# Kernel tuning notes

Measured on AMD Instinct MI355X. Metric: run time of the kernel, lower is better.

## Reference

```python
import jax, jax.numpy as jnp
import numpy as np

NB = 2        # trm_num_blocks
H = 4         # trm_num_heads
D = 128       # trm_hidden_dim
L = 512
B = 1
PAD = 0
NEG = jnp.float32(-2**32 + 1)


def _ln(x, g, b, eps=1e-8):
    m = x.mean(-1, keepdims=True)
    v = x.var(-1, keepdims=True)
    return (x - m) / jnp.sqrt(v + eps) * g + b


def setup_inputs() -> dict:
    key = jax.random.key(0)
    ks = jax.random.split(key, 16)
    s = 0.02
    inp = {
        "log_seqs": jax.random.randint(ks[0], (B, L), 0, 1000),
        "seqs": jax.random.normal(ks[1], (B, L, D), jnp.float32),
        "time_matrix_K": jax.random.normal(ks[2], (B, L, L, D), jnp.float32),
        # per-block stacked params [NB, ...]
        "Wq": jax.random.normal(ks[3], (NB, D, D), jnp.float32) * s,
        "bq": jnp.zeros((NB, D), jnp.float32),
        "Wk": jax.random.normal(ks[4], (NB, D, D), jnp.float32) * s,
        "bk": jnp.zeros((NB, D), jnp.float32),
        "Wv": jax.random.normal(ks[5], (NB, D, D), jnp.float32) * s,
        "bv": jnp.zeros((NB, D), jnp.float32),
        "Wt": jax.random.normal(ks[6], (NB, D, D), jnp.float32) * s,
        "bt": jnp.zeros((NB, D), jnp.float32),
        "Wtp": jax.random.normal(ks[7], (NB, D, 1), jnp.float32) * s,
        "btp": jnp.zeros((NB, 1), jnp.float32),
        "ln1_g": jnp.ones((NB, D), jnp.float32),
        "ln1_b": jnp.zeros((NB, D), jnp.float32),
        "ln2_g": jnp.ones((NB, D), jnp.float32),
        "ln2_b": jnp.zeros((NB, D), jnp.float32),
        "W1": jax.random.normal(ks[8], (NB, D, D), jnp.float32) * s,
        "b1": jnp.zeros((NB, D), jnp.float32),
        "W2": jax.random.normal(ks[9], (NB, D, D), jnp.float32) * s,
        "b2": jnp.zeros((NB, D), jnp.float32),
        "lnf_g": jnp.ones((D,), jnp.float32),
        "lnf_b": jnp.zeros((D,), jnp.float32),
    }
    return inp


def reference(log_seqs, seqs, time_matrix_K, Wq, bq, Wk, bk, Wv, bv, Wt, bt,
              Wtp, btp, ln1_g, ln1_b, ln2_g, ln2_b, W1, b1, W2, b2, lnf_g, lnf_b):
    hd = D // H
    pad = (log_seqs == PAD)                     # [B, L] True at padding
    keep = (~pad)[..., None].astype(seqs.dtype)  # [B, L, 1]
    seqs = seqs * keep
    causal = ~jnp.tril(jnp.ones((L, L), bool))  # True above diagonal (masked)
    # combined mask [1, B, L, L]: pad query rows OR non-causal entries
    mask = pad[None, :, :, None] | causal[None, None, :, :]

    attn_ws = []
    for i in range(NB):
        Q = _ln(seqs, ln1_g[i], ln1_b[i])
        q = Q @ Wq[i] + bq[i]
        k = seqs @ Wk[i] + bk[i]
        v = seqs @ Wv[i] + bv[i]
        # head-major layout [H, B, L, hd] (matches torch split+cat along dim 0)
        qh = q.reshape(B, L, H, hd).transpose(2, 0, 1, 3)
        kh = k.reshape(B, L, H, hd).transpose(2, 0, 1, 3)
        vh = v.reshape(B, L, H, hd).transpose(2, 0, 1, 3)
        scores = jnp.einsum('hbqd,hbkd->hbqk', qh, kh)  # [H, B, L, L]
        # time bias: sigmoid(proj(relu(W_t t))) in (0,1); log is negative
        tw = jax.nn.sigmoid(
            (jax.nn.relu(time_matrix_K @ Wt[i] + bt[i]) @ Wtp[i] + btp[i]).squeeze(-1)
        )                                             # [B, L, L]
        scores = (scores + jnp.log(tw)) / jnp.float32(hd) ** 0.5
        scores = jnp.where(mask, NEG, scores)
        w = jax.nn.softmax(scores, axis=-1)           # dropout is identity (eval)
        attn_ws.append(w.reshape(H * B, L, L))
        out = jnp.einsum('hbqk,hbkd->hbqd', w, vh).transpose(1, 2, 0, 3).reshape(B, L, D)
        seqs = Q + out
        x = _ln(seqs, ln2_g[i], ln2_b[i])
        y = jax.nn.relu(x @ W1[i] + b1[i]) @ W2[i] + b2[i]
        seqs = (x + y) * keep                         # FFN residual adds post-LN x
    log_feats = _ln(seqs, lnf_g, lnf_b)
    return (log_feats, tuple(attn_ws))
```

## Files before the change

kernel.cpp:

```cpp
#include <hip/hip_runtime.h>

#define L 512
#define D 128
#define H 4
#define HD 32
#define XLD 132

typedef __bf16 bf16x8 __attribute__((ext_vector_type(8)));
typedef float  f32x4  __attribute__((ext_vector_type(4)));

__device__ __forceinline__ unsigned short bfbits(float v){
  __bf16 h = (__bf16)v; unsigned short u; __builtin_memcpy(&u, &h, 2); return u;
}
__device__ __forceinline__ bf16x8 cvt8(float4 a0, float4 a1){
  bf16x8 r;
  r[0] = (__bf16)a0.x; r[1] = (__bf16)a0.y; r[2] = (__bf16)a0.z; r[3] = (__bf16)a0.w;
  r[4] = (__bf16)a1.x; r[5] = (__bf16)a1.y; r[6] = (__bf16)a1.z; r[7] = (__bf16)a1.w;
  return r;
}

__device__ __forceinline__ void write_qA(unsigned short* qA, int row, int c, float v){
  int qt = row >> 4, m = row & 15;
  int h = c >> 5, cc = c & 31;
  qA[(((qt * 4 + h) * 64) + (cc >> 3) * 16 + m) * 8 + (cc & 7)] = bfbits(v);
}
__device__ __forceinline__ void write_kB(unsigned short* kB, int row, int c, float v){
  int h = c >> 5, cc = c & 31;
  int nt = row >> 4;
  kB[((h * 32 + nt) * 64 + (cc >> 3) * 16 + (row & 15)) * 8 + (cc & 7)] = bfbits(v);
}
__device__ __forceinline__ void write_vB(unsigned short* vB, int row, int c, float v){
  int h = c >> 5, cc = c & 31;
  int kk = row >> 5, qv = (row >> 3) & 3, jv = row & 7;
  int nt = cc >> 4;
  vB[(((h * 16 + kk) * 2 + nt) * 64 + qv * 16 + (cc & 15)) * 8 + jv] = bfbits(v);
}

__device__ __forceinline__ void row_stats16(const float (*buf)[XLD], int tid,
                                            float* mean_s, float* rstd_s){
  int row_l = tid >> 4, seg = tid & 15;
  const float* p = &buf[row_l][seg * 8];
  float4 f0 = *(const float4*)p, f1 = *(const float4*)(p + 4);
  float sum = f0.x + f0.y + f0.z + f0.w + f1.x + f1.y + f1.z + f1.w;
  float sq  = f0.x*f0.x + f0.y*f0.y + f0.z*f0.z + f0.w*f0.w
            + f1.x*f1.x + f1.y*f1.y + f1.z*f1.z + f1.w*f1.w;
#pragma unroll
  for (int o = 1; o < 16; o <<= 1){ sum += __shfl_xor(sum, o); sq += __shfl_xor(sq, o); }
  if (seg == 0){
    float mn = sum * (1.f / 128.f);
    mean_s[row_l] = mn;
    rstd_s[row_l] = rsqrtf(fmaxf(sq * (1.f / 128.f) - mn * mn, 0.f) + 1e-8f);
  }
}

__device__ __forceinline__ void build_afr(const float (*buf)[XLD], int lane, bf16x8* afr){
  int m = lane & 15, quad = lane >> 4;
#pragma unroll
  for (int k0 = 0; k0 < 4; ++k0){
    const float* p = &buf[m][k0 * 32 + quad * 8];
    afr[k0] = cvt8(*(const float4*)p, *(const float4*)(p + 4));
  }
}
__device__ __forceinline__ void build_afr_ln(const float (*buf)[XLD], int lane,
    const float* mean_s, const float* rstd_s,
    const float* __restrict__ g, const float* __restrict__ b, bf16x8* afr){
  int m = lane & 15, quad = lane >> 4;
  float mn = mean_s[m], rs = rstd_s[m];
#pragma unroll
  for (int k0 = 0; k0 < 4; ++k0){
    int c0 = k0 * 32 + quad * 8;
    const float* p = &buf[m][c0];
    float4 a0 = *(const float4*)p, a1 = *(const float4*)(p + 4);
    float q[8];
    q[0]=(a0.x-mn)*rs*g[c0+0]+b[c0+0]; q[1]=(a0.y-mn)*rs*g[c0+1]+b[c0+1];
    q[2]=(a0.z-mn)*rs*g[c0+2]+b[c0+2]; q[3]=(a0.w-mn)*rs*g[c0+3]+b[c0+3];
    q[4]=(a1.x-mn)*rs*g[c0+4]+b[c0+4]; q[5]=(a1.y-mn)*rs*g[c0+5]+b[c0+5];
    q[6]=(a1.z-mn)*rs*g[c0+6]+b[c0+6]; q[7]=(a1.w-mn)*rs*g[c0+7]+b[c0+7];
    bf16x8 r;
    r[0]=(__bf16)q[0]; r[1]=(__bf16)q[1]; r[2]=(__bf16)q[2]; r[3]=(__bf16)q[3];
    r[4]=(__bf16)q[4]; r[5]=(__bf16)q[5]; r[6]=(__bf16)q[6]; r[7]=(__bf16)q[7];
    afr[k0] = r;
  }
}

__global__ void k_prep(const float* __restrict__ Wt,
                       const float* __restrict__ Wq, const float* __restrict__ Wk,
                       const float* __restrict__ Wv, const float* __restrict__ W1,
                       const float* __restrict__ W2,
                       unsigned short* __restrict__ bfg, unsigned short* __restrict__ wf){
  int idx = blockIdx.x * 256 + threadIdx.x;
  if (idx < 32768){
    int jj   = idx & 7;
    int lane = (idx >> 3) & 63;
    int k0   = (idx >> 9) & 3;
    int nt   = idx >> 11;
    int d    = k0 * 32 + (lane >> 4) * 8 + jj;
    int col  = (nt & 7) * 16 + (lane & 15);
    int blk  = nt >> 3;
    bfg[idx] = bfbits(Wt[blk * D * D + d * D + col]);
  } else {
    int i2 = idx - 32768;
    int jj = i2 & 7, lane = (i2 >> 3) & 63, k0 = (i2 >> 9) & 3, nt = (i2 >> 11) & 7;
    int mat = i2 >> 14;
    int blk = mat / 5, m5 = mat % 5;
    const float* W = (m5 == 0 ? Wq : m5 == 1 ? Wk : m5 == 2 ? Wv : m5 == 3 ? W1 : W2)
                     + blk * D * D;
    int d = k0 * 32 + (lane >> 4) * 8 + jj;
    int col = nt * 16 + (lane & 15);
    wf[i2] = bfbits(W[d * D + col]);
  }
}

__global__ __launch_bounds__(256, 4) void k_timebias(
    const float* __restrict__ T, const unsigned short* __restrict__ bfg,
    const float* __restrict__ bt, const float* __restrict__ wtp,
    const float* __restrict__ btp, float* __restrict__ logtw){
  __shared__ __align__(16) unsigned short bsh[16384];
  __shared__ float bts[128], wtps[128];
  int tid = threadIdx.x;
  int lane = tid & 63, w = tid >> 6;
  int quad = lane >> 4, m = lane & 15;
  const bf16x8* bls = (const bf16x8*)bsh;
  int wbase = blockIdx.x * 256 + w * 64;

  bf16x8 afr[4][4];
#pragma unroll
  for (int mt = 0; mt < 4; ++mt){
    const float* tp = T + (size_t)(wbase + mt * 16 + m) * D + quad * 8;
#pragma unroll
    for (int k0 = 0; k0 < 4; ++k0){
      float4 f0 = *(const float4*)(tp + k0 * 32);
      float4 f1 = *(const float4*)(tp + k0 * 32 + 4);
      afr[mt][k0] = cvt8(f0, f1);
    }
  }

#pragma unroll
  for (int blk = 0; blk < 2; ++blk){
    if (blk) __syncthreads();
    {
      const uint4* g = (const uint4*)(bfg + blk * 16384);
      uint4* s = (uint4*)bsh;
#pragma unroll
      for (int i = 0; i < 8; ++i) s[tid + i * 256] = g[tid + i * 256];
      if (tid < 128){ bts[tid] = bt[blk * 128 + tid]; wtps[tid] = wtp[blk * 128 + tid]; }
    }
    __syncthreads();

    f32x4 rs[4] = {{0,0,0,0},{0,0,0,0},{0,0,0,0},{0,0,0,0}};
#pragma unroll
    for (int ntl = 0; ntl < 8; ++ntl){
      f32x4 acc[4] = {{0,0,0,0},{0,0,0,0},{0,0,0,0},{0,0,0,0}};
#pragma unroll
      for (int k0 = 0; k0 < 4; ++k0){
        bf16x8 b = bls[(ntl * 4 + k0) * 64 + lane];
#pragma unroll
        for (int mt = 0; mt < 4; ++mt)
          acc[mt] = __builtin_amdgcn_mfma_f32_16x16x32_bf16(afr[mt][k0], b, acc[mt], 0, 0, 0);
      }
      float btv = bts[ntl * 16 + m];
      float wtv = wtps[ntl * 16 + m];
#pragma unroll
      for (int mt = 0; mt < 4; ++mt)
#pragma unroll
        for (int r = 0; r < 4; ++r)
          rs[mt][r] += fmaxf(acc[mt][r] + btv, 0.f) * wtv;
    }
#pragma unroll
    for (int mt = 0; mt < 4; ++mt)
#pragma unroll
      for (int r = 0; r < 4; ++r){
        float v = rs[mt][r];
        v += __shfl_xor(v, 1); v += __shfl_xor(v, 2);
        v += __shfl_xor(v, 4); v += __shfl_xor(v, 8);
        rs[mt][r] = v;
      }
    if (m == 0){
      float bp = btp[blk];
      float* out = logtw + blk * (L * L);
#pragma unroll
      for (int mt = 0; mt < 4; ++mt){
        float4 o;
        float s0 = rs[mt][0] + bp; o.x = -logf(1.f + expf(-s0));
        float s1 = rs[mt][1] + bp; o.y = -logf(1.f + expf(-s1));
        float s2 = rs[mt][2] + bp; o.z = -logf(1.f + expf(-s2));
        float s3 = rs[mt][3] + bp; o.w = -logf(1.f + expf(-s3));
        *(float4*)(out + wbase + mt * 16 + quad * 4) = o;
      }
    }
  }
}

__global__ __launch_bounds__(256) void k_qkv_m(
    const float* __restrict__ src, const int* __restrict__ ls, int domask,
    const float* __restrict__ g1, const float* __restrict__ b1,
    const unsigned short* __restrict__ wf, int matq,
    const float* __restrict__ bq, const float* __restrict__ bk,
    const float* __restrict__ bv,
    float* __restrict__ Q, unsigned short* __restrict__ qA,
    unsigned short* __restrict__ kB, unsigned short* __restrict__ vB){
  __shared__ float xs[16][XLD];
  __shared__ float mean_s[16], rstd_s[16];
  __shared__ float g1s[128], b1s[128];
  int tid = threadIdx.x, rowbase = blockIdx.x * 16;
  int row_l = tid >> 4, seg = tid & 15;

  const float* sp = src + (rowbase + row_l) * D + seg * 8;
  float4 f0 = *(const float4*)sp, f1 = *(const float4*)(sp + 4);
  if (domask && ls[rowbase + row_l] == 0){
    f0 = make_float4(0,0,0,0); f1 = make_float4(0,0,0,0);
  }
  *(float4*)&xs[row_l][seg * 8] = f0;
  *(float4*)&xs[row_l][seg * 8 + 4] = f1;
  if (tid < 128){ g1s[tid] = g1[tid]; b1s[tid] = b1[tid]; }
  __syncthreads();
  row_stats16(xs, tid, mean_s, rstd_s);
  __syncthreads();

  {
    float mn = mean_s[row_l], rs = rstd_s[row_l];
    float* qp = Q + (rowbase + row_l) * D + seg * 8;
    float4 o0, o1;
    int c0 = seg * 8;
    o0.x=(f0.x-mn)*rs*g1s[c0+0]+b1s[c0+0]; o0.y=(f0.y-mn)*rs*g1s[c0+1]+b1s[c0+1];
    o0.z=(f0.z-mn)*rs*g1s[c0+2]+b1s[c0+2]; o0.w=(f0.w-mn)*rs*g1s[c0+3]+b1s[c0+3];
    o1.x=(f1.x-mn)*rs*g1s[c0+4]+b1s[c0+4]; o1.y=(f1.y-mn)*rs*g1s[c0+5]+b1s[c0+5];
    o1.z=(f1.z-mn)*rs*g1s[c0+6]+b1s[c0+6]; o1.w=(f1.w-mn)*rs*g1s[c0+7]+b1s[c0+7];
    *(float4*)qp = o0; *(float4*)(qp + 4) = o1;
  }

  int lane = tid & 63, w = tid >> 6;
  int quad = lane >> 4, mcol = lane & 15;
  bf16x8 afrQ[4], afrX[4];
  build_afr_ln(xs, lane, mean_s, rstd_s, g1s, b1s, afrQ);
  build_afr(xs, lane, afrX);

#pragma unroll
  for (int jl = 0; jl < 6; ++jl){
    int j = w * 6 + jl;
    int mat = j >> 3, nt = j & 7;
    const bf16x8* wfb = (const bf16x8*)wf + ((size_t)(matq + mat) * 8 + nt) * 4 * 64;
    f32x4 acc = {0, 0, 0, 0};
#pragma unroll
    for (int k0 = 0; k0 < 4; ++k0)
      acc = __builtin_amdgcn_mfma_f32_16x16x32_bf16(mat == 0 ? afrQ[k0] : afrX[k0],
                                                    wfb[k0 * 64 + lane], acc, 0, 0, 0);
    int c = nt * 16 + mcol;
    float bias = (mat == 0 ? bq : mat == 1 ? bk : bv)[c];
#pragma unroll
    for (int r = 0; r < 4; ++r){
      int row = rowbase + quad * 4 + r;
      float v = acc[r] + bias;
      if (mat == 0) write_qA(qA, row, c, v);
      else if (mat == 1) write_kB(kB, row, c, v);
      else write_vB(vB, row, c, v);
    }
  }
}

__global__ __launch_bounds__(256) void k_attn(
    const unsigned short* __restrict__ qA, const unsigned short* __restrict__ kB,
    const unsigned short* __restrict__ vB, const float* __restrict__ logtw,
    const int* __restrict__ ls, const float* __restrict__ Q,
    float* __restrict__ wout, float* __restrict__ xr){
  __shared__ __align__(16) unsigned short pa[16 * 64 * 8];
  __shared__ float pvp[4][2][64][4];
  __shared__ float smax[4][16], ssum[4][16];
  int qt = blockIdx.x >> 2, h = blockIdx.x & 3;
  int tid = threadIdx.x, lane = tid & 63, w = tid >> 6;
  int quad = lane >> 4, mcol = lane & 15;
  const float RS = 0.17677669529663687f;

  bf16x8 qf = ((const bf16x8*)qA)[(qt * 4 + h) * 64 + lane];

  f32x4 acc[8];
#pragma unroll
  for (int nt8 = 0; nt8 < 8; ++nt8){
    bf16x8 bf = ((const bf16x8*)kB)[(h * 32 + w * 8 + nt8) * 64 + lane];
    f32x4 z = {0, 0, 0, 0};
    acc[nt8] = __builtin_amdgcn_mfma_f32_16x16x32_bf16(qf, bf, z, 0, 0, 0);
  }

  float e[8][4];
  float mx4[4] = {-3e38f, -3e38f, -3e38f, -3e38f};
#pragma unroll
  for (int nt8 = 0; nt8 < 8; ++nt8){
    int col = w * 128 + nt8 * 16 + mcol;
#pragma unroll
    for (int r = 0; r < 4; ++r){
      int row = qt * 16 + quad * 4 + r;
      float sv = (acc[nt8][r] + logtw[row * L + col]) * RS;
      sv = (col <= row) ? sv : -3e38f;
      e[nt8][r] = sv;
      mx4[r] = fmaxf(mx4[r], sv);
    }
  }
#pragma unroll
  for (int r = 0; r < 4; ++r){
    float v = mx4[r];
    v = fmaxf(v, __shfl_xor(v, 1)); v = fmaxf(v, __shfl_xor(v, 2));
    v = fmaxf(v, __shfl_xor(v, 4)); v = fmaxf(v, __shfl_xor(v, 8));
    mx4[r] = v;
  }
  if (mcol == 0){
#pragma unroll
    for (int r = 0; r < 4; ++r) smax[w][quad * 4 + r] = mx4[r];
  }
  __syncthreads();
  float mxr[4], sum4[4] = {0, 0, 0, 0};
#pragma unroll
  for (int r = 0; r < 4; ++r){
    int rr = quad * 4 + r;
    mxr[r] = fmaxf(fmaxf(smax[0][rr], smax[1][rr]), fmaxf(smax[2][rr], smax[3][rr]));
  }
#pragma unroll
  for (int nt8 = 0; nt8 < 8; ++nt8)
#pragma unroll
    for (int r = 0; r < 4; ++r){
      float sv = e[nt8][r];
      float ev = (sv > -1e38f) ? expf(sv - mxr[r]) : 0.f;
      e[nt8][r] = ev;
      sum4[r] += ev;
    }
#pragma unroll
  for (int r = 0; r < 4; ++r){
    float v = sum4[r];
    v += __shfl_xor(v, 1); v += __shfl_xor(v, 2);
    v += __shfl_xor(v, 4); v += __shfl_xor(v, 8);
    sum4[r] = v;
  }
  if (mcol == 0){
#pragma unroll
    for (int r = 0; r < 4; ++r) ssum[w][quad * 4 + r] = sum4[r];
  }
  __syncthreads();
  float inv[4]; int padr[4];
#pragma unroll
  for (int r = 0; r < 4; ++r){
    int rr = quad * 4 + r;
    inv[r] = 1.f / (ssum[0][rr] + ssum[1][rr] + ssum[2][rr] + ssum[3][rr]);
    padr[r] = (ls[qt * 16 + rr] == 0);
  }
#pragma unroll
  for (int nt8 = 0; nt8 < 8; ++nt8){
    int col = w * 128 + nt8 * 16 + mcol;
    int kk = col >> 5, qk = (col >> 3) & 3, jj = col & 7;
#pragma unroll
    for (int r = 0; r < 4; ++r){
      int rl = quad * 4 + r;
      float wv = padr[r] ? (1.f / 512.f) : e[nt8][r] * inv[r];
      wout[h * (L * L) + (qt * 16 + rl) * L + col] = wv;
      pa[(kk * 64 + qk * 16 + rl) * 8 + jj] = bfbits(wv);
    }
  }

  f32x4 pacc[2] = {{0,0,0,0},{0,0,0,0}};
#pragma unroll
  for (int kk4 = 0; kk4 < 4; ++kk4){
    int kk = w * 4 + kk4;
    bf16x8 af = ((const bf16x8*)pa)[kk * 64 + lane];
#pragma unroll
    for (int nt = 0; nt < 2; ++nt){
      bf16x8 bf = ((const bf16x8*)vB)[((h * 16 + kk) * 2 + nt) * 64 + lane];
      pacc[nt] = __builtin_amdgcn_mfma_f32_16x16x32_bf16(af, bf, pacc[nt], 0, 0, 0);
    }
  }
#pragma unroll
  for (int nt = 0; nt < 2; ++nt)
#pragma unroll
    for (int r = 0; r < 4; ++r) pvp[w][nt][lane][r] = pacc[nt][r];
  __syncthreads();
  if (w < 2){
    int nt = w;
#pragma unroll
    for (int r = 0; r < 4; ++r){
      float o = pvp[0][nt][lane][r] + pvp[1][nt][lane][r]
              + pvp[2][nt][lane][r] + pvp[3][nt][lane][r];
      int row = qt * 16 + quad * 4 + r;
      int cg = h * HD + nt * 16 + mcol;
      xr[row * D + cg] = Q[row * D + cg] + o;
    }
  }
}

__global__ __launch_bounds__(256) void k_ffn_m(
    const float* __restrict__ xr, const int* __restrict__ ls,
    const float* __restrict__ g2, const float* __restrict__ b2,
    const unsigned short* __restrict__ wf, int mat1,
    const float* __restrict__ b1f, const float* __restrict__ b2f,
    int fuse_qkv, const float* __restrict__ g1, const float* __restrict__ b1,
    int matq, const float* __restrict__ bq, const float* __restrict__ bk,
    const float* __restrict__ bv,
    float* __restrict__ Q, unsigned short* __restrict__ qA,
    unsigned short* __restrict__ kB, unsigned short* __restrict__ vB,
    int fuse_lnf, const float* __restrict__ lg, const float* __restrict__ lb,
    float* __restrict__ lf){
  __shared__ float xs[16][XLD];
  __shared__ float x2s[16][XLD];
  __shared__ float y1s[16][XLD];
  __shared__ float xos[16][XLD];
  __shared__ float mean_s[16], rstd_s[16];
  __shared__ float gs[128], bs[128];
  int tid = threadIdx.x, rowbase = blockIdx.x * 16;
  int row_l = tid >> 4, seg = tid & 15;
  int lane = tid & 63, w = tid >> 6;
  int quad = lane >> 4, mcol = lane & 15;

  {
    const float* sp = xr + (rowbase + row_l) * D + seg * 8;
    *(float4*)&xs[row_l][seg * 8] = *(const float4*)sp;
    *(float4*)&xs[row_l][seg * 8 + 4] = *(const float4*)(sp + 4);
    if (tid < 128){ gs[tid] = g2[tid]; bs[tid] = b2[tid]; }
  }
  __syncthreads();
  row_stats16(xs, tid, mean_s, rstd_s);
  __syncthreads();
  {
    float mn = mean_s[row_l], rs = rstd_s[row_l];
#pragma unroll
    for (int i = 0; i < 8; ++i){
      int c = seg * 8 + i;
      x2s[row_l][c] = (xs[row_l][c] - mn) * rs * gs[c] + bs[c];
    }
  }
  __syncthreads();

  bf16x8 afr[4];
  build_afr(x2s, lane, afr);
#pragma unroll
  for (int jl = 0; jl < 2; ++jl){
    int nt = w * 2 + jl;
    const bf16x8* wfb = (const bf16x8*)wf + ((size_t)mat1 * 8 + nt) * 4 * 64;
    f32x4 acc = {0, 0, 0, 0};
#pragma unroll
    for (int k0 = 0; k0 < 4; ++k0)
      acc = __builtin_amdgcn_mfma_f32_16x16x32_bf16(afr[k0], wfb[k0 * 64 + lane], acc, 0, 0, 0);
    int c = nt * 16 + mcol;
    float bias = b1f[c];
#pragma unroll
    for (int r = 0; r < 4; ++r)
      y1s[quad * 4 + r][c] = fmaxf(acc[r] + bias, 0.f);
  }
  __syncthreads();

  build_afr(y1s, lane, afr);
#pragma unroll
  for (int jl = 0; jl < 2; ++jl){
    int nt = w * 2 + jl;
    const bf16x8* wfb = (const bf16x8*)wf + ((size_t)(mat1 + 1) * 8 + nt) * 4 * 64;
    f32x4 acc = {0, 0, 0, 0};
#pragma unroll
    for (int k0 = 0; k0 < 4; ++k0)
      acc = __builtin_amdgcn_mfma_f32_16x16x32_bf16(afr[k0], wfb[k0 * 64 + lane], acc, 0, 0, 0);
    int c = nt * 16 + mcol;
    float bias = b2f[c];
#pragma unroll
    for (int r = 0; r < 4; ++r){
      int rl = quad * 4 + r;
      float kp = (ls[rowbase + rl] != 0) ? 1.f : 0.f;
      xos[rl][c] = (x2s[rl][c] + acc[r] + bias) * kp;
    }
  }
  __syncthreads();

  if (fuse_qkv){
    if (tid < 128){ gs[tid] = g1[tid]; bs[tid] = b1[tid]; }
    row_stats16(xos, tid, mean_s, rstd_s);
    __syncthreads();
    {
      float mn = mean_s[row_l], rs = rstd_s[row_l];
      float* qp = Q + (rowbase + row_l) * D + seg * 8;
      float4 o0, o1;
      int c0 = seg * 8;
      o0.x=(xos[row_l][c0+0]-mn)*rs*gs[c0+0]+bs[c0+0];
      o0.y=(xos[row_l][c0+1]-mn)*rs*gs[c0+1]+bs[c0+1];
      o0.z=(xos[row_l][c0+2]-mn)*rs*gs[c0+2]+bs[c0+2];
      o0.w=(xos[row_l][c0+3]-mn)*rs*gs[c0+3]+bs[c0+3];
      o1.x=(xos[row_l][c0+4]-mn)*rs*gs[c0+4]+bs[c0+4];
      o1.y=(xos[row_l][c0+5]-mn)*rs*gs[c0+5]+bs[c0+5];
      o1.z=(xos[row_l][c0+6]-mn)*rs*gs[c0+6]+bs[c0+6];
      o1.w=(xos[row_l][c0+7]-mn)*rs*gs[c0+7]+bs[c0+7];
      *(float4*)qp = o0; *(float4*)(qp + 4) = o1;
    }
    bf16x8 afrQ[4], afrX[4];
    build_afr_ln(xos, lane, mean_s, rstd_s, gs, bs, afrQ);
    build_afr(xos, lane, afrX);
#pragma unroll
    for (int jl = 0; jl < 6; ++jl){
      int j = w * 6 + jl;
      int mat = j >> 3, nt = j & 7;
      const bf16x8* wfb = (const bf16x8*)wf + ((size_t)(matq + mat) * 8 + nt) * 4 * 64;
      f32x4 acc = {0, 0, 0, 0};
#pragma unroll
      for (int k0 = 0; k0 < 4; ++k0)
        acc = __builtin_amdgcn_mfma_f32_16x16x32_bf16(mat == 0 ? afrQ[k0] : afrX[k0],
                                                      wfb[k0 * 64 + lane], acc, 0, 0, 0);
      int c = nt * 16 + mcol;
      float bias = (mat == 0 ? bq : mat == 1 ? bk : bv)[c];
#pragma unroll
      for (int r = 0; r < 4; ++r){
        int row = rowbase + quad * 4 + r;
        float v = acc[r] + bias;
        if (mat == 0) write_qA(qA, row, c, v);
        else if (mat == 1) write_kB(kB, row, c, v);
        else write_vB(vB, row, c, v);
      }
    }
  }

  if (fuse_lnf){
    if (tid < 128){ gs[tid] = lg[tid]; bs[tid] = lb[tid]; }
    row_stats16(xos, tid, mean_s, rstd_s);
    __syncthreads();
    float mn = mean_s[row_l], rs = rstd_s[row_l];
    float* op = lf + (rowbase + row_l) * D + seg * 8;
    float4 o0, o1;
    int c0 = seg * 8;
    o0.x=(xos[row_l][c0+0]-mn)*rs*gs[c0+0]+bs[c0+0];
    o0.y=(xos[row_l][c0+1]-mn)*rs*gs[c0+1]+bs[c0+1];
    o0.z=(xos[row_l][c0+2]-mn)*rs*gs[c0+2]+bs[c0+2];
    o0.w=(xos[row_l][c0+3]-mn)*rs*gs[c0+3]+bs[c0+3];
    o1.x=(xos[row_l][c0+4]-mn)*rs*gs[c0+4]+bs[c0+4];
    o1.y=(xos[row_l][c0+5]-mn)*rs*gs[c0+5]+bs[c0+5];
    o1.z=(xos[row_l][c0+6]-mn)*rs*gs[c0+6]+bs[c0+6];
    o1.w=(xos[row_l][c0+7]-mn)*rs*gs[c0+7]+bs[c0+7];
    *(float4*)op = o0; *(float4*)(op + 4) = o1;
  }
}

extern "C" void kernel_launch(void* const* d_in, const int* in_sizes, int n_in,
                              void* d_out, int out_size, void* d_ws, size_t ws_size,
                              hipStream_t stream){
  const int*   ls   = (const int*)d_in[0];
  const float* seqs = (const float*)d_in[1];
  const float* T    = (const float*)d_in[2];
  const float* Wq   = (const float*)d_in[3];
  const float* bq   = (const float*)d_in[4];
  const float* Wk   = (const float*)d_in[5];
  const float* bk   = (const float*)d_in[6];
  const float* Wv   = (const float*)d_in[7];
  const float* bv   = (const float*)d_in[8];
  const float* Wt   = (const float*)d_in[9];
  const float* bt   = (const float*)d_in[10];
  const float* Wtp  = (const float*)d_in[11];
  const float* btp  = (const float*)d_in[12];
  const float* g1   = (const float*)d_in[13];
  const float* b1   = (const float*)d_in[14];
  const float* g2   = (const float*)d_in[15];
  const float* b2   = (const float*)d_in[16];
  const float* W1   = (const float*)d_in[17];
  const float* b1f  = (const float*)d_in[18];
  const float* W2   = (const float*)d_in[19];
  const float* b2f  = (const float*)d_in[20];
  const float* lg   = (const float*)d_in[21];
  const float* lb   = (const float*)d_in[22];

  float* ws    = (float*)d_ws;
  float* Q     = ws;
  float* xr    = Q + 65536;
  float* logtw = xr + 65536;
  unsigned short* bfg = (unsigned short*)(logtw + 2 * 262144);
  unsigned short* wf  = bfg + 32768;
  unsigned short* qA  = wf + 163840;
  unsigned short* kB  = qA + 65536;
  unsigned short* vB  = kB + 65536;

  float* outF = (float*)d_out;
  float* lf = outF;
  float* w0 = outF + 65536;
  float* w1 = w0 + 1048576;

  k_prep    <<<768, 256, 0, stream>>>(Wt, Wq, Wk, Wv, W1, W2, bfg, wf);
  k_timebias<<<1024, 256, 0, stream>>>(T, bfg, bt, Wtp, btp, logtw);

  k_qkv_m<<<32, 256, 0, stream>>>(seqs, ls, 1, g1, b1, wf, 0, bq, bk, bv,
                                  Q, qA, kB, vB);
  k_attn<<<128, 256, 0, stream>>>(qA, kB, vB, logtw, ls, Q, w0, xr);
  k_ffn_m<<<32, 256, 0, stream>>>(xr, ls, g2, b2, wf, 3, b1f, b2f,
                                  1, g1 + D, b1 + D, 5, bq + D, bk + D, bv + D,
                                  Q, qA, kB, vB,
                                  0, lg, lb, lf);
  k_attn<<<128, 256, 0, stream>>>(qA, kB, vB, logtw + L * L, ls, Q, w1, xr);
  k_ffn_m<<<32, 256, 0, stream>>>(xr, ls, g2 + D, b2 + D, wf, 8, b1f + D, b2f + D,
                                  0, g1, b1, 0, bq, bk, bv,
                                  Q, qA, kB, vB,
                                  1, lg, lb, lf);
}
```

Measured before the change: 299.1 us.

## Split QKV projection across grid y, use fast exp/log intrinsics, relax timebias occupancy

The first QKV kernel now launches a 32x3 grid, so each block handles only one of Q, K or V instead of all three. This triples the block count for better GPU fill. The softplus in the time-bias kernel and the softmax exp in attention switch to the fast __expf/__logf intrinsics, trading some precision for cheaper transcendentals. The time-bias launch bound's minimum blocks-per-CU hint drops from 4 to 2, giving the compiler more registers per thread at the cost of possible occupancy.

```diff
diff --git a/kernel.cpp b/kernel.cpp
--- a/kernel.cpp
+++ b/kernel.cpp
@@ -111,7 +111,7 @@
   }
 }
 
-__global__ __launch_bounds__(256, 4) void k_timebias(
+__global__ __launch_bounds__(256, 2) void k_timebias(
     const float* __restrict__ T, const unsigned short* __restrict__ bfg,
     const float* __restrict__ bt, const float* __restrict__ wtp,
     const float* __restrict__ btp, float* __restrict__ logtw){
@@ -181,10 +181,10 @@
 #pragma unroll
       for (int mt = 0; mt < 4; ++mt){
         float4 o;
-        float s0 = rs[mt][0] + bp; o.x = -logf(1.f + expf(-s0));
-        float s1 = rs[mt][1] + bp; o.y = -logf(1.f + expf(-s1));
-        float s2 = rs[mt][2] + bp; o.z = -logf(1.f + expf(-s2));
-        float s3 = rs[mt][3] + bp; o.w = -logf(1.f + expf(-s3));
+        float s0 = rs[mt][0] + bp; o.x = -__logf(1.f + __expf(-s0));
+        float s1 = rs[mt][1] + bp; o.y = -__logf(1.f + __expf(-s1));
+        float s2 = rs[mt][2] + bp; o.z = -__logf(1.f + __expf(-s2));
+        float s3 = rs[mt][3] + bp; o.w = -__logf(1.f + __expf(-s3));
         *(float4*)(out + wbase + mt * 16 + quad * 4) = o;
       }
     }
@@ -203,6 +203,7 @@
   __shared__ float mean_s[16], rstd_s[16];
   __shared__ float g1s[128], b1s[128];
   int tid = threadIdx.x, rowbase = blockIdx.x * 16;
+  int mat = blockIdx.y;
   int row_l = tid >> 4, seg = tid & 15;
 
   const float* sp = src + (rowbase + row_l) * D + seg * 8;
@@ -212,12 +213,11 @@
   }
   *(float4*)&xs[row_l][seg * 8] = f0;
   *(float4*)&xs[row_l][seg * 8 + 4] = f1;
-  if (tid < 128){ g1s[tid] = g1[tid]; b1s[tid] = b1[tid]; }
-  __syncthreads();
-  row_stats16(xs, tid, mean_s, rstd_s);
-  __syncthreads();
-
-  {
+  if (mat == 0 && tid < 128){ g1s[tid] = g1[tid]; b1s[tid] = b1[tid]; }
+  __syncthreads();
+  if (mat == 0){
+    row_stats16(xs, tid, mean_s, rstd_s);
+    __syncthreads();
     float mn = mean_s[row_l], rs = rstd_s[row_l];
     float* qp = Q + (rowbase + row_l) * D + seg * 8;
     float4 o0, o1;
@@ -231,22 +231,21 @@
 
   int lane = tid & 63, w = tid >> 6;
   int quad = lane >> 4, mcol = lane & 15;
-  bf16x8 afrQ[4], afrX[4];
-  build_afr_ln(xs, lane, mean_s, rstd_s, g1s, b1s, afrQ);
-  build_afr(xs, lane, afrX);
-
-#pragma unroll
-  for (int jl = 0; jl < 6; ++jl){
-    int j = w * 6 + jl;
-    int mat = j >> 3, nt = j & 7;
+  bf16x8 afr[4];
+  if (mat == 0) build_afr_ln(xs, lane, mean_s, rstd_s, g1s, b1s, afr);
+  else          build_afr(xs, lane, afr);
+
+  const float* bias_v = (mat == 0 ? bq : mat == 1 ? bk : bv);
+#pragma unroll
+  for (int jl = 0; jl < 2; ++jl){
+    int nt = w * 2 + jl;
     const bf16x8* wfb = (const bf16x8*)wf + ((size_t)(matq + mat) * 8 + nt) * 4 * 64;
     f32x4 acc = {0, 0, 0, 0};
 #pragma unroll
     for (int k0 = 0; k0 < 4; ++k0)
-      acc = __builtin_amdgcn_mfma_f32_16x16x32_bf16(mat == 0 ? afrQ[k0] : afrX[k0],
-                                                    wfb[k0 * 64 + lane], acc, 0, 0, 0);
+      acc = __builtin_amdgcn_mfma_f32_16x16x32_bf16(afr[k0], wfb[k0 * 64 + lane], acc, 0, 0, 0);
     int c = nt * 16 + mcol;
-    float bias = (mat == 0 ? bq : mat == 1 ? bk : bv)[c];
+    float bias = bias_v[c];
 #pragma unroll
     for (int r = 0; r < 4; ++r){
       int row = rowbase + quad * 4 + r;
@@ -318,7 +317,7 @@
 #pragma unroll
     for (int r = 0; r < 4; ++r){
       float sv = e[nt8][r];
-      float ev = (sv > -1e38f) ? expf(sv - mxr[r]) : 0.f;
+      float ev = (sv > -1e38f) ? __expf(sv - mxr[r]) : 0.f;
       e[nt8][r] = ev;
       sum4[r] += ev;
     }
@@ -573,8 +572,8 @@
   k_prep    <<<768, 256, 0, stream>>>(Wt, Wq, Wk, Wv, W1, W2, bfg, wf);
   k_timebias<<<1024, 256, 0, stream>>>(T, bfg, bt, Wtp, btp, logtw);
 
-  k_qkv_m<<<32, 256, 0, stream>>>(seqs, ls, 1, g1, b1, wf, 0, bq, bk, bv,
-                                  Q, qA, kB, vB);
+  k_qkv_m<<<dim3(32, 3), 256, 0, stream>>>(seqs, ls, 1, g1, b1, wf, 0, bq, bk, bv,
+                                           Q, qA, kB, vB);
   k_attn<<<128, 256, 0, stream>>>(qA, kB, vB, logtw, ls, Q, w0, xr);
   k_ffn_m<<<32, 256, 0, stream>>>(xr, ls, g2, b2, wf, 3, b1f, b2f,
                                   1, g1 + D, b1 + D, 5, bq + D, bk + D, bv + D,
```

After: 276.6 us. 7.5% less time.
